# Optimization experiments

Measured on AMD Instinct MI355X. Metric: run time of the kernel, lower is better.

## Reference

```python
import jax, jax.numpy as jnp
import numpy as np

N_NODES = 50000
N_EDGES = 800000
IN_F = 191
H1, C1 = 16, 16   # conv1: heads=16, out=16, concat -> 256
H2, C2 = 8, 3     # conv2: heads=8, out=3, concat=False -> mean


def _glorot(key, shape):
    fan = shape[0] + shape[-1] if len(shape) == 2 else sum(shape)
    s = jnp.sqrt(6.0 / fan)
    return jax.random.uniform(key, shape, jnp.float32, -s, s)


def setup_inputs() -> dict:
    key = jax.random.key(0)
    ks = jax.random.split(key, 16)
    x = jax.random.normal(ks[0], (N_NODES, IN_F), jnp.float32)
    edge_index = jax.random.randint(ks[1], (2, N_EDGES), 0, N_NODES)
    edge_attr = jax.random.normal(ks[2], (N_EDGES, 1), jnp.float32)
    return {
        "x": x, "edge_index": edge_index, "edge_attr": edge_attr,
        "W1": _glorot(ks[3], (IN_F, H1 * C1)),
        "We1": _glorot(ks[4], (1, H1 * C1)),
        "a_src1": _glorot(ks[5], (H1, C1)),
        "a_dst1": _glorot(ks[6], (H1, C1)),
        "a_edge1": _glorot(ks[7], (H1, C1)),
        "b1": jnp.zeros((H1 * C1,), jnp.float32),
        "W2": _glorot(ks[8], (H1 * C1, H2 * C2)),
        "We2": _glorot(ks[9], (1, H2 * C2)),
        "a_src2": _glorot(ks[10], (H2, C2)),
        "a_dst2": _glorot(ks[11], (H2, C2)),
        "a_edge2": _glorot(ks[12], (H2, C2)),
        "b2": jnp.zeros((C2,), jnp.float32),
    }


def gat_conv(x, src, dst, edge_attr, W, We, a_src, a_dst, a_edge, bias, H, C, concat):
    # x: [N, F]; src/dst: [E'] (self loops already appended); edge_attr: [E', De]
    N = x.shape[0]
    xl = (x @ W).reshape(N, H, C)                       # [N,H,C]
    e = (edge_attr @ We).reshape(-1, H, C)              # [E',H,C]
    alpha_src = (xl * a_src).sum(-1)                    # [N,H]
    alpha_dst = (xl * a_dst).sum(-1)                    # [N,H]
    alpha_e = (e * a_edge).sum(-1)                      # [E',H]
    alpha = alpha_src[src] + alpha_dst[dst] + alpha_e   # [E',H]
    alpha = jax.nn.leaky_relu(alpha, 0.2)
    # softmax over incoming edges per destination node
    m = jax.ops.segment_max(alpha, dst, num_segments=N)
    alpha = jnp.exp(alpha - m[dst])
    den = jax.ops.segment_sum(alpha, dst, num_segments=N)
    alpha = alpha / (den[dst] + 1e-16)
    out = jax.ops.segment_sum(alpha[:, :, None] * xl[src], dst, num_segments=N)  # [N,H,C]
    if concat:
        return out.reshape(N, H * C) + bias
    return out.mean(axis=1) + bias


def reference(x, edge_index, edge_attr, W1, We1, a_src1, a_dst1, a_edge1, b1,
              W2, We2, a_src2, a_dst2, a_edge2, b2):
    N = x.shape[0]
    # add self loops (PyG default, edge_attr fill_value='mean')
    loop = jnp.arange(N)
    src = jnp.concatenate([edge_index[0], loop])
    dst = jnp.concatenate([edge_index[1], loop])
    ea_mean = edge_attr.mean(axis=0, keepdims=True)
    ea = jnp.concatenate([edge_attr, jnp.broadcast_to(ea_mean, (N, edge_attr.shape[1]))], axis=0)

    h = gat_conv(x, src, dst, ea, W1, We1, a_src1, a_dst1, a_edge1, b1, H1, C1, True)
    h = jax.nn.elu(h)
    h = gat_conv(h, src, dst, ea, W2, We2, a_src2, a_dst2, a_edge2, b2, H2, C2, False)
    h = jax.nn.elu(h)
    return h
```

## Files before the change

kernel.cpp:

```cpp
#include <hip/hip_runtime.h>
#include <math.h>
#include <stdint.h>

#define N_NODES 50000
#define N_EDGES 800000
#define N_TOT   850000
#define IN_F    191
#define F1      256
#define NH1     16
#define NC1     16
#define F2      24
#define NH2     8
#define NC2     3
#define KP      192
#define MPAD    50048
#define NCVT_X  (MPAD * 24)
#define NCVT_W  (F1 * 24)

typedef __attribute__((ext_vector_type(8))) short bf16x8;
typedef __attribute__((ext_vector_type(4))) float f32x4;

#define GLL16(g, s) __builtin_amdgcn_global_load_lds( \
    (const __attribute__((address_space(1))) void*)(g), \
    (__attribute__((address_space(3))) void*)(s), 16, 0, 0)

__device__ __forceinline__ float lrelu(float x) { return x > 0.f ? x : 0.2f * x; }

__device__ __forceinline__ uint16_t f2bf1(float f) {
    uint32_t u = __float_as_uint(f);
    return (uint16_t)((u + 0x7fffu + ((u >> 16) & 1u)) >> 16);
}
__device__ __forceinline__ void bf2f2(uint32_t u, float* lo, float* hi) {
    *lo = __uint_as_float(u << 16);
    *hi = __uint_as_float(u & 0xffff0000u);
}

__global__ void k_hist(const int* __restrict__ ei, int* counts) {
    int e = blockIdx.x * blockDim.x + threadIdx.x;
    if (e < N_EDGES) atomicAdd(&counts[ei[N_EDGES + e]], 1);
}

__global__ void k_easum(const float* __restrict__ ea, float* __restrict__ part) {
    __shared__ float wsums[4];
    int t = threadIdx.x;
    float v = 0.f;
    for (int e = blockIdx.x * 256 + t; e < N_EDGES; e += 256 * 256) v += ea[e];
    #pragma unroll
    for (int off = 32; off >= 1; off >>= 1) v += __shfl_xor(v, off);
    if ((t & 63) == 0) wsums[t >> 6] = v;
    __syncthreads();
    if (t == 0) part[blockIdx.x] = wsums[0] + wsums[1] + wsums[2] + wsums[3];
}

__global__ void k_wedot(const float* __restrict__ We1, const float* __restrict__ ae1,
                        const float* __restrict__ We2, const float* __restrict__ ae2,
                        const float* __restrict__ part, float* scalars) {
    int t = threadIdx.x;
    if (t < NH1) {
        float s = 0.f;
        for (int c = 0; c < NC1; c++) s += We1[t * NC1 + c] * ae1[t * NC1 + c];
        scalars[1 + t] = s;
    } else if (t < NH1 + NH2) {
        int h = t - NH1;
        float s = 0.f;
        for (int c = 0; c < NC2; c++) s += We2[h * NC2 + c] * ae2[h * NC2 + c];
        scalars[17 + h] = s;
    }
    float v = part[t * 4] + part[t * 4 + 1] + part[t * 4 + 2] + part[t * 4 + 3];
    #pragma unroll
    for (int off = 32; off >= 1; off >>= 1) v += __shfl_xor(v, off);
    if (t == 0) scalars[0] = v / (float)N_EDGES;
}

__global__ __launch_bounds__(1024) void k_scan1(const int* __restrict__ counts,
                                                int* rowptr, int* bsums) {
    __shared__ int wsum[16];
    int t = threadIdx.x;
    int lane = t & 63, w = t >> 6;
    int i = blockIdx.x * 1024 + t;
    int v = (i < N_NODES) ? counts[i] + 1 : 0;
    int incl = v;
    #pragma unroll
    for (int off = 1; off < 64; off <<= 1) {
        int u = __shfl_up(incl, off);
        if (lane >= off) incl += u;
    }
    if (lane == 63) wsum[w] = incl;
    __syncthreads();
    int woff = 0;
    #pragma unroll
    for (int k = 0; k < 16; k++) woff += (k < w) ? wsum[k] : 0;
    if (i < N_NODES) rowptr[i] = woff + incl - v;
    if (t == 1023) bsums[blockIdx.x] = woff + incl;
}

__global__ __launch_bounds__(1024) void k_scan2(int* rowptr, int* cursor,
                                                const int* __restrict__ bsums) {
    __shared__ int off_s;
    int b = blockIdx.x, t = threadIdx.x;
    if (t == 0) {
        int o = 0;
        for (int k = 0; k < b; k++) o += bsums[k];
        off_s = o;
        if (b == 48) rowptr[N_NODES] = o + bsums[48];
    }
    __syncthreads();
    int i = b * 1024 + t;
    if (i < N_NODES) {
        int r = rowptr[i] + off_s;
        rowptr[i] = r;
        cursor[i] = r;
    }
}

__global__ void k_scatter(const int* __restrict__ ei, const float* __restrict__ ea,
                          const float* __restrict__ scalars, int* cursor,
                          uint32_t* __restrict__ csr) {
    int i = blockIdx.x * blockDim.x + threadIdx.x;
    if (i < N_EDGES) {
        int s = ei[i], d = ei[N_EDGES + i];
        int pos = atomicAdd(&cursor[d], 1);
        csr[pos] = (uint32_t)s | ((uint32_t)f2bf1(ea[i]) << 16);
    } else if (i < N_TOT) {
        int n = i - N_EDGES;
        int pos = atomicAdd(&cursor[n], 1);
        csr[pos] = (uint32_t)n | ((uint32_t)f2bf1(scalars[0]) << 16);
    }
}

__global__ void k_cvt(const float* __restrict__ x, const float* __restrict__ W1,
                      uint16_t* __restrict__ xh, uint16_t* __restrict__ wht) {
    int idx = blockIdx.x * 256 + threadIdx.x;
    if (idx < NCVT_X) {
        int row = idx / 24, kw = idx - row * 24;
        int k0 = kw * 8;
        uint16_t hv[8];
        #pragma unroll
        for (int j = 0; j < 8; j++) {
            int k = k0 + j;
            float v = (row < N_NODES && k < IN_F) ? x[(size_t)row * IN_F + k] : 0.f;
            hv[j] = f2bf1(v);
        }
        *(uint4*)(xh + (size_t)row * KP + k0) = *(const uint4*)hv;
    } else if (idx < NCVT_X + NCVT_W) {
        int id2 = idx - NCVT_X;
        int col = id2 / 24, kw = id2 - col * 24;
        int k0 = kw * 8;
        uint16_t hv[8];
        #pragma unroll
        for (int j = 0; j < 8; j++) {
            int k = k0 + j;
            float v = (k < IN_F) ? W1[(size_t)k * F1 + col] : 0.f;
            hv[j] = f2bf1(v);
        }
        *(uint4*)(wht + (size_t)col * KP + k0) = *(const uint4*)hv;
    }
}

__global__ __launch_bounds__(256) void k_gemm1_mfma(const uint16_t* __restrict__ xh,
        const uint16_t* __restrict__ wht, uint16_t* __restrict__ xl1b) {
    __shared__ uint16_t ldsA[8 * 64 * 8];
    __shared__ uint16_t ldsB[8 * 64 * 8];
    const int t = threadIdx.x;
    const int l = t & 63, w = t >> 6;
    const int wm = w >> 1, wn = w & 1;
    const int m0 = blockIdx.x * 128;
    const int n0 = blockIdx.y * 128;
    const int lr = l & 15, lk = l >> 4;

    f32x4 acc[4][4];
    #pragma unroll
    for (int i = 0; i < 4; i++)
        #pragma unroll
        for (int j = 0; j < 4; j++)
            acc[i][j] = (f32x4){0.f, 0.f, 0.f, 0.f};

    for (int ks = 0; ks < 6; ks++) {
        const int kb = ks * 32 + lk * 8;
        #pragma unroll
        for (int ii = 0; ii < 4; ii++) {
            const int idx = w * 4 + ii;
            if (idx < 8) {
                const uint16_t* src = xh + (size_t)(m0 + idx * 16 + lr) * KP + kb;
                GLL16(src, ldsA + idx * 512);
            } else {
                const int g = idx - 8;
                const uint16_t* src = wht + (size_t)(n0 + g * 16 + lr) * KP + kb;
                GLL16(src, ldsB + g * 512);
            }
        }
        __syncthreads();
        bf16x8 ah[4];
        #pragma unroll
        for (int i = 0; i < 4; i++)
            ah[i] = *(const bf16x8*)(ldsA + ((wm * 4 + i) * 64 + l) * 8);
        #pragma unroll
        for (int j = 0; j < 4; j++) {
            bf16x8 bh = *(const bf16x8*)(ldsB + ((wn * 4 + j) * 64 + l) * 8);
            #pragma unroll
            for (int i = 0; i < 4; i++)
                acc[i][j] = __builtin_amdgcn_mfma_f32_16x16x32_bf16(ah[i], bh, acc[i][j], 0, 0, 0);
        }
        __syncthreads();
    }
    #pragma unroll
    for (int i = 0; i < 4; i++) {
        const int gm_base = m0 + wm * 64 + i * 16 + lk * 4;
        #pragma unroll
        for (int r = 0; r < 4; r++) {
            const int gm = gm_base + r;
            if (gm < N_NODES) {
                #pragma unroll
                for (int j = 0; j < 4; j++) {
                    const int gn = n0 + wn * 64 + j * 16 + lr;
                    xl1b[(size_t)gm * F1 + gn] = f2bf1(acc[i][j][r]);
                }
            }
        }
    }
}

__global__ void k_alphas1(const uint16_t* __restrict__ xl1b, const float* __restrict__ a_src,
                          const float* __restrict__ a_dst,
                          float* __restrict__ asrc, float* __restrict__ adst) {
    int idx = blockIdx.x * blockDim.x + threadIdx.x;
    if (idx >= N_NODES * NH1) return;
    int h = idx & 15;
    const uint4* xp = (const uint4*)(xl1b + (size_t)idx * 16);
    uint4 u0 = xp[0], u1 = xp[1];
    uint32_t us[8] = {u0.x, u0.y, u0.z, u0.w, u1.x, u1.y, u1.z, u1.w};
    float as = 0.f, ad = 0.f;
    #pragma unroll
    for (int q = 0; q < 8; q++) {
        float lo, hi;
        bf2f2(us[q], &lo, &hi);
        as += lo * a_src[h * 16 + 2 * q] + hi * a_src[h * 16 + 2 * q + 1];
        ad += lo * a_dst[h * 16 + 2 * q] + hi * a_dst[h * 16 + 2 * q + 1];
    }
    asrc[idx] = as;
    adst[idx] = ad;
}

__global__ __launch_bounds__(256) void k_agg1(const int* __restrict__ rowptr,
        const uint32_t* __restrict__ csr,
        const uint16_t* __restrict__ xl1b, const float* __restrict__ asrc,
        const float* __restrict__ adst, const float* __restrict__ scalars,
        const float* __restrict__ b1, uint16_t* __restrict__ h1b) {
    int node = blockIdx.x * 4 + (threadIdx.x >> 6);
    int lane = threadIdx.x & 63;
    int eg = lane >> 4, h = lane & 15;
    int r0 = rowptr[node], r1 = rowptr[node + 1];
    float ad = adst[node * 16 + h];
    float wd = scalars[1 + h];
    float den = 0.f;
    float acc[16];
    #pragma unroll
    for (int c = 0; c < 16; c++) acc[c] = 0.f;
    for (int j = r0 + eg; j < r1; j += 4) {
        uint32_t pk = csr[j];
        int s = (int)(pk & 0xFFFFu);
        float eav = __uint_as_float(pk & 0xFFFF0000u);
        float a = lrelu(asrc[s * 16 + h] + ad + eav * wd);
        float wgt = __expf(a);
        den += wgt;
        const uint4* xp = (const uint4*)(xl1b + (size_t)s * F1 + h * 16);
        uint4 u0 = xp[0], u1 = xp[1];
        float lo, hi;
        bf2f2(u0.x, &lo, &hi); acc[0] += wgt * lo;  acc[1] += wgt * hi;
        bf2f2(u0.y, &lo, &hi); acc[2] += wgt * lo;  acc[3] += wgt * hi;
        bf2f2(u0.z, &lo, &hi); acc[4] += wgt * lo;  acc[5] += wgt * hi;
        bf2f2(u0.w, &lo, &hi); acc[6] += wgt * lo;  acc[7] += wgt * hi;
        bf2f2(u1.x, &lo, &hi); acc[8] += wgt * lo;  acc[9] += wgt * hi;
        bf2f2(u1.y, &lo, &hi); acc[10] += wgt * lo; acc[11] += wgt * hi;
        bf2f2(u1.z, &lo, &hi); acc[12] += wgt * lo; acc[13] += wgt * hi;
        bf2f2(u1.w, &lo, &hi); acc[14] += wgt * lo; acc[15] += wgt * hi;
    }
    den += __shfl_xor(den, 16);
    den += __shfl_xor(den, 32);
    float inv = 1.f / (den + 1e-16f);
    #pragma unroll
    for (int c = 0; c < 16; c++) {
        acc[c] += __shfl_xor(acc[c], 16);
        acc[c] += __shfl_xor(acc[c], 32);
    }
    if (eg == 0) {
        uint32_t pk[8];
        #pragma unroll
        for (int q = 0; q < 8; q++) {
            float v0 = acc[2 * q] * inv + b1[h * 16 + 2 * q];
            float v1 = acc[2 * q + 1] * inv + b1[h * 16 + 2 * q + 1];
            v0 = v0 > 0.f ? v0 : expm1f(v0);
            v1 = v1 > 0.f ? v1 : expm1f(v1);
            pk[q] = (uint32_t)f2bf1(v0) | ((uint32_t)f2bf1(v1) << 16);
        }
        uint4* op = (uint4*)(h1b + (size_t)node * F1 + h * 16);
        op[0] = make_uint4(pk[0], pk[1], pk[2], pk[3]);
        op[1] = make_uint4(pk[4], pk[5], pk[6], pk[7]);
    }
}

__global__ __launch_bounds__(256) void k_layer2(const uint16_t* __restrict__ h1b,
        const float* __restrict__ W2, const float* __restrict__ a_src,
        const float* __restrict__ a_dst, uint16_t* __restrict__ xl2b,
        float* __restrict__ asrc, float* __restrict__ adst) {
    __shared__ float W2s[F2][258];
    int t = threadIdx.x;
    for (int i = t; i < 256 * F2; i += 256) {
        int k = i / F2, c = i - k * F2;
        W2s[c][k] = W2[i];
    }
    __syncthreads();
    int idx = blockIdx.x * 256 + t;
    if (idx >= N_NODES * NH2) return;
    int n = idx >> 3, h = idx & 7;
    int c0 = h * 3;
    const uint4* hp = (const uint4*)(h1b + (size_t)n * F1);
    float a0 = 0.f, a1 = 0.f, a2 = 0.f;
    #pragma unroll 4
    for (int q = 0; q < 32; q++) {
        uint4 u = hp[q];
        float f[8];
        bf2f2(u.x, &f[0], &f[1]);
        bf2f2(u.y, &f[2], &f[3]);
        bf2f2(u.z, &f[4], &f[5]);
        bf2f2(u.w, &f[6], &f[7]);
        #pragma unroll
        for (int j = 0; j < 8; j++) {
            int k = q * 8 + j;
            a0 += f[j] * W2s[c0][k];
            a1 += f[j] * W2s[c0 + 1][k];
            a2 += f[j] * W2s[c0 + 2][k];
        }
    }
    uint2 pk;
    pk.x = (uint32_t)f2bf1(a0) | ((uint32_t)f2bf1(a1) << 16);
    pk.y = (uint32_t)f2bf1(a2);
    *(uint2*)(xl2b + (size_t)idx * 4) = pk;
    asrc[idx] = a0 * a_src[h * 3 + 0] + a1 * a_src[h * 3 + 1] + a2 * a_src[h * 3 + 2];
    adst[idx] = a0 * a_dst[h * 3 + 0] + a1 * a_dst[h * 3 + 1] + a2 * a_dst[h * 3 + 2];
}

__global__ __launch_bounds__(256) void k_agg2(const int* __restrict__ rowptr,
        const uint32_t* __restrict__ csr,
        const uint16_t* __restrict__ xl2b, const float* __restrict__ asrc,
        const float* __restrict__ adst, const float* __restrict__ scalars,
        const float* __restrict__ b2, float* __restrict__ out) {
    int node = blockIdx.x * 4 + (threadIdx.x >> 6);
    int lane = threadIdx.x & 63;
    int eg = lane >> 3, h = lane & 7;
    int r0 = rowptr[node], r1 = rowptr[node + 1];
    float ad = adst[node * 8 + h];
    float wd = scalars[17 + h];
    float den = 0.f, a0 = 0.f, a1 = 0.f, a2 = 0.f;
    for (int j = r0 + eg; j < r1; j += 8) {
        uint32_t pk = csr[j];
        int s = (int)(pk & 0xFFFFu);
        float eav = __uint_as_float(pk & 0xFFFF0000u);
        float a = lrelu(asrc[s * 8 + h] + ad + eav * wd);
        float wgt = __expf(a);
        den += wgt;
        const uint2* xp = (const uint2*)(xl2b + ((size_t)s * 8 + h) * 4);
        uint2 u = xp[0];
        float x0, x1, x2, dummy;
        bf2f2(u.x, &x0, &x1);
        bf2f2(u.y, &x2, &dummy);
        a0 += wgt * x0;
        a1 += wgt * x1;
        a2 += wgt * x2;
    }
    den += __shfl_xor(den, 8); den += __shfl_xor(den, 16); den += __shfl_xor(den, 32);
    float inv = 1.f / (den + 1e-16f);
    a0 += __shfl_xor(a0, 8); a0 += __shfl_xor(a0, 16); a0 += __shfl_xor(a0, 32);
    a1 += __shfl_xor(a1, 8); a1 += __shfl_xor(a1, 16); a1 += __shfl_xor(a1, 32);
    a2 += __shfl_xor(a2, 8); a2 += __shfl_xor(a2, 16); a2 += __shfl_xor(a2, 32);
    a0 *= inv; a1 *= inv; a2 *= inv;
    a0 += __shfl_xor(a0, 1); a0 += __shfl_xor(a0, 2); a0 += __shfl_xor(a0, 4);
    a1 += __shfl_xor(a1, 1); a1 += __shfl_xor(a1, 2); a1 += __shfl_xor(a1, 4);
    a2 += __shfl_xor(a2, 1); a2 += __shfl_xor(a2, 2); a2 += __shfl_xor(a2, 4);
    if (lane == 0) {
        float v0 = a0 * 0.125f + b2[0];
        float v1 = a1 * 0.125f + b2[1];
        float v2 = a2 * 0.125f + b2[2];
        out[node * 3 + 0] = v0 > 0.f ? v0 : expm1f(v0);
        out[node * 3 + 1] = v1 > 0.f ? v1 : expm1f(v1);
        out[node * 3 + 2] = v2 > 0.f ? v2 : expm1f(v2);
    }
}

extern "C" void kernel_launch(void* const* d_in, const int* in_sizes, int n_in,
                              void* d_out, int out_size, void* d_ws, size_t ws_size,
                              hipStream_t stream) {
    const float* x       = (const float*)d_in[0];
    const int*   ei      = (const int*)d_in[1];
    const float* ea      = (const float*)d_in[2];
    const float* W1      = (const float*)d_in[3];
    const float* We1     = (const float*)d_in[4];
    const float* a_src1  = (const float*)d_in[5];
    const float* a_dst1  = (const float*)d_in[6];
    const float* a_edge1 = (const float*)d_in[7];
    const float* b1      = (const float*)d_in[8];
    const float* W2      = (const float*)d_in[9];
    const float* We2     = (const float*)d_in[10];
    const float* a_src2  = (const float*)d_in[11];
    const float* a_dst2  = (const float*)d_in[12];
    const float* a_edge2 = (const float*)d_in[13];
    const float* b2      = (const float*)d_in[14];
    float* out = (float*)d_out;

    char* ws = (char*)d_ws;
    size_t off = 0;
    auto alloc = [&](size_t nbytes) -> void* {
        void* p = ws + off;
        off = (off + nbytes + 255) & ~(size_t)255;
        return p;
    };
    uint16_t* xl1b  = (uint16_t*)alloc((size_t)N_NODES * F1 * 2);
    uint16_t* h1b   = (uint16_t*)alloc((size_t)N_NODES * F1 * 2);
    float* asrc1    = (float*)alloc((size_t)N_NODES * NH1 * 4);
    float* adst1    = (float*)alloc((size_t)N_NODES * NH1 * 4);
    uint16_t* xl2b  = (uint16_t*)alloc((size_t)N_NODES * 32 * 2);
    float* asrc2    = (float*)alloc((size_t)N_NODES * NH2 * 4);
    float* adst2    = (float*)alloc((size_t)N_NODES * NH2 * 4);
    int*   counts   = (int*)alloc((size_t)N_NODES * 4);
    int*   rowptr   = (int*)alloc((size_t)(N_NODES + 1) * 4);
    int*   cursor   = (int*)alloc((size_t)N_NODES * 4);
    int*   bsums    = (int*)alloc(64 * 4);
    uint32_t* csr   = (uint32_t*)alloc((size_t)N_TOT * 4);
    float* scalars  = (float*)alloc(128);
    float* part     = (float*)alloc(256 * 4);
    uint16_t* wht   = (uint16_t*)alloc((size_t)F1 * KP * 2);
    uint16_t* xh    = (uint16_t*)alloc((size_t)MPAD * KP * 2);

    hipMemsetAsync(counts, 0, (size_t)N_NODES * 4, stream);
    hipLaunchKernelGGL(k_hist, dim3((N_EDGES + 255) / 256), dim3(256), 0, stream,
                       ei, counts);
    hipLaunchKernelGGL(k_easum, dim3(256), dim3(256), 0, stream, ea, part);
    hipLaunchKernelGGL(k_wedot, dim3(1), dim3(64), 0, stream,
                       We1, a_edge1, We2, a_edge2, part, scalars);
    hipLaunchKernelGGL(k_scan1, dim3(49), dim3(1024), 0, stream, counts, rowptr, bsums);
    hipLaunchKernelGGL(k_scan2, dim3(49), dim3(1024), 0, stream, rowptr, cursor, bsums);
    hipLaunchKernelGGL(k_scatter, dim3((N_TOT + 255) / 256), dim3(256), 0, stream,
                       ei, ea, scalars, cursor, csr);
    hipLaunchKernelGGL(k_cvt, dim3((NCVT_X + NCVT_W + 255) / 256), dim3(256), 0, stream,
                       x, W1, xh, wht);
    hipLaunchKernelGGL(k_gemm1_mfma, dim3(MPAD / 128, 2), dim3(256), 0, stream,
                       xh, wht, xl1b);
    hipLaunchKernelGGL(k_alphas1, dim3((N_NODES * NH1 + 255) / 256), dim3(256), 0, stream,
                       xl1b, a_src1, a_dst1, asrc1, adst1);
    hipLaunchKernelGGL(k_agg1, dim3(N_NODES / 4), dim3(256), 0, stream,
                       rowptr, csr, xl1b, asrc1, adst1, scalars, b1, h1b);
    hipLaunchKernelGGL(k_layer2, dim3((N_NODES * NH2 + 255) / 256), dim3(256), 0, stream,
                       h1b, W2, a_src2, a_dst2, xl2b, asrc2, adst2);
    hipLaunchKernelGGL(k_agg2, dim3(N_NODES / 4), dim3(256), 0, stream,
                       rowptr, csr, xl2b, asrc2, adst2, scalars, b2, out);
}
```

Before: 296.3 us.

## Fuse preprocessing kernels and fold attention-logit computation into GEMM epilogue

Merges the histogram, edge-attr sum and bf16 conversion kernels into one launch. It also folds the scalar We·a_edge and mean computation into an extra block of the scan kernel. The GEMM is retiled to 64 rows by the full 256 columns per block, so each block holds whole node rows. The tile is staged in LDS so the per-head source/destination attention dots are computed in the epilogue, which removes the separate k_alphas1 pass that re-read xl1b. This cuts launch count and global traffic, at the cost of 32KB of LDS per block and a different GEMM tile shape that may lower occupancy.

```diff
diff --git a/kernel.cpp b/kernel.cpp
--- a/kernel.cpp
+++ b/kernel.cpp
@@ -16,6 +16,9 @@
 #define MPAD    50048
 #define NCVT_X  (MPAD * 24)
 #define NCVT_W  (F1 * 24)
+#define HIST_B  3125
+#define EASUM_B 256
+#define CVT_B   ((NCVT_X + NCVT_W) / 256)
 
 typedef __attribute__((ext_vector_type(8))) short bf16x8;
 typedef __attribute__((ext_vector_type(4))) float f32x4;
@@ -35,49 +38,81 @@
     *hi = __uint_as_float(u & 0xffff0000u);
 }
 
-__global__ void k_hist(const int* __restrict__ ei, int* counts) {
-    int e = blockIdx.x * blockDim.x + threadIdx.x;
-    if (e < N_EDGES) atomicAdd(&counts[ei[N_EDGES + e]], 1);
-}
-
-__global__ void k_easum(const float* __restrict__ ea, float* __restrict__ part) {
-    __shared__ float wsums[4];
-    int t = threadIdx.x;
-    float v = 0.f;
-    for (int e = blockIdx.x * 256 + t; e < N_EDGES; e += 256 * 256) v += ea[e];
-    #pragma unroll
-    for (int off = 32; off >= 1; off >>= 1) v += __shfl_xor(v, off);
-    if ((t & 63) == 0) wsums[t >> 6] = v;
-    __syncthreads();
-    if (t == 0) part[blockIdx.x] = wsums[0] + wsums[1] + wsums[2] + wsums[3];
-}
-
-__global__ void k_wedot(const float* __restrict__ We1, const float* __restrict__ ae1,
-                        const float* __restrict__ We2, const float* __restrict__ ae2,
-                        const float* __restrict__ part, float* scalars) {
-    int t = threadIdx.x;
-    if (t < NH1) {
-        float s = 0.f;
-        for (int c = 0; c < NC1; c++) s += We1[t * NC1 + c] * ae1[t * NC1 + c];
-        scalars[1 + t] = s;
-    } else if (t < NH1 + NH2) {
-        int h = t - NH1;
-        float s = 0.f;
-        for (int c = 0; c < NC2; c++) s += We2[h * NC2 + c] * ae2[h * NC2 + c];
-        scalars[17 + h] = s;
-    }
-    float v = part[t * 4] + part[t * 4 + 1] + part[t * 4 + 2] + part[t * 4 + 3];
-    #pragma unroll
-    for (int off = 32; off >= 1; off >>= 1) v += __shfl_xor(v, off);
-    if (t == 0) scalars[0] = v / (float)N_EDGES;
+__global__ void k_pre(const int* __restrict__ ei, const float* __restrict__ ea,
+                      const float* __restrict__ x, const float* __restrict__ W1,
+                      int* counts, float* __restrict__ part,
+                      uint16_t* __restrict__ xh, uint16_t* __restrict__ wht) {
+    int b = blockIdx.x, t = threadIdx.x;
+    if (b < HIST_B) {
+        int e = b * 256 + t;
+        if (e < N_EDGES) atomicAdd(&counts[ei[N_EDGES + e]], 1);
+    } else if (b < HIST_B + EASUM_B) {
+        __shared__ float wsums[4];
+        int eb = b - HIST_B;
+        float v = 0.f;
+        for (int e = eb * 256 + t; e < N_EDGES; e += 256 * 256) v += ea[e];
+        #pragma unroll
+        for (int off = 32; off >= 1; off >>= 1) v += __shfl_xor(v, off);
+        if ((t & 63) == 0) wsums[t >> 6] = v;
+        __syncthreads();
+        if (t == 0) part[eb] = wsums[0] + wsums[1] + wsums[2] + wsums[3];
+    } else {
+        int idx = (b - HIST_B - EASUM_B) * 256 + t;
+        if (idx < NCVT_X) {
+            int row = idx / 24, kw = idx - row * 24;
+            int k0 = kw * 8;
+            uint16_t hv[8];
+            #pragma unroll
+            for (int j = 0; j < 8; j++) {
+                int k = k0 + j;
+                float v = (row < N_NODES && k < IN_F) ? x[(size_t)row * IN_F + k] : 0.f;
+                hv[j] = f2bf1(v);
+            }
+            *(uint4*)(xh + (size_t)row * KP + k0) = *(const uint4*)hv;
+        } else {
+            int id2 = idx - NCVT_X;
+            int col = id2 / 24, kw = id2 - col * 24;
+            int k0 = kw * 8;
+            uint16_t hv[8];
+            #pragma unroll
+            for (int j = 0; j < 8; j++) {
+                int k = k0 + j;
+                float v = (k < IN_F) ? W1[(size_t)k * F1 + col] : 0.f;
+                hv[j] = f2bf1(v);
+            }
+            *(uint4*)(wht + (size_t)col * KP + k0) = *(const uint4*)hv;
+        }
+    }
 }
 
 __global__ __launch_bounds__(1024) void k_scan1(const int* __restrict__ counts,
-                                                int* rowptr, int* bsums) {
+        int* rowptr, int* bsums,
+        const float* __restrict__ We1, const float* __restrict__ ae1,
+        const float* __restrict__ We2, const float* __restrict__ ae2,
+        const float* __restrict__ part, float* scalars) {
+    int b = blockIdx.x, t = threadIdx.x;
+    if (b == 49) {
+        if (t < 64) {
+            if (t < NH1) {
+                float s = 0.f;
+                for (int c = 0; c < NC1; c++) s += We1[t * NC1 + c] * ae1[t * NC1 + c];
+                scalars[1 + t] = s;
+            } else if (t < NH1 + NH2) {
+                int h = t - NH1;
+                float s = 0.f;
+                for (int c = 0; c < NC2; c++) s += We2[h * NC2 + c] * ae2[h * NC2 + c];
+                scalars[17 + h] = s;
+            }
+            float v = part[t * 4] + part[t * 4 + 1] + part[t * 4 + 2] + part[t * 4 + 3];
+            #pragma unroll
+            for (int off = 32; off >= 1; off >>= 1) v += __shfl_xor(v, off);
+            if (t == 0) scalars[0] = v / (float)N_EDGES;
+        }
+        return;
+    }
     __shared__ int wsum[16];
-    int t = threadIdx.x;
     int lane = t & 63, w = t >> 6;
-    int i = blockIdx.x * 1024 + t;
+    int i = b * 1024 + t;
     int v = (i < N_NODES) ? counts[i] + 1 : 0;
     int incl = v;
     #pragma unroll
@@ -91,7 +126,7 @@
     #pragma unroll
     for (int k = 0; k < 16; k++) woff += (k < w) ? wsum[k] : 0;
     if (i < N_NODES) rowptr[i] = woff + incl - v;
-    if (t == 1023) bsums[blockIdx.x] = woff + incl;
+    if (t == 1023) bsums[b] = woff + incl;
 }
 
 __global__ __launch_bounds__(1024) void k_scan2(int* rowptr, int* cursor,
@@ -128,44 +163,16 @@
     }
 }
 
-__global__ void k_cvt(const float* __restrict__ x, const float* __restrict__ W1,
-                      uint16_t* __restrict__ xh, uint16_t* __restrict__ wht) {
-    int idx = blockIdx.x * 256 + threadIdx.x;
-    if (idx < NCVT_X) {
-        int row = idx / 24, kw = idx - row * 24;
-        int k0 = kw * 8;
-        uint16_t hv[8];
-        #pragma unroll
-        for (int j = 0; j < 8; j++) {
-            int k = k0 + j;
-            float v = (row < N_NODES && k < IN_F) ? x[(size_t)row * IN_F + k] : 0.f;
-            hv[j] = f2bf1(v);
-        }
-        *(uint4*)(xh + (size_t)row * KP + k0) = *(const uint4*)hv;
-    } else if (idx < NCVT_X + NCVT_W) {
-        int id2 = idx - NCVT_X;
-        int col = id2 / 24, kw = id2 - col * 24;
-        int k0 = kw * 8;
-        uint16_t hv[8];
-        #pragma unroll
-        for (int j = 0; j < 8; j++) {
-            int k = k0 + j;
-            float v = (k < IN_F) ? W1[(size_t)k * F1 + col] : 0.f;
-            hv[j] = f2bf1(v);
-        }
-        *(uint4*)(wht + (size_t)col * KP + k0) = *(const uint4*)hv;
-    }
-}
-
 __global__ __launch_bounds__(256) void k_gemm1_mfma(const uint16_t* __restrict__ xh,
-        const uint16_t* __restrict__ wht, uint16_t* __restrict__ xl1b) {
-    __shared__ uint16_t ldsA[8 * 64 * 8];
-    __shared__ uint16_t ldsB[8 * 64 * 8];
+        const uint16_t* __restrict__ wht, const float* __restrict__ a_src,
+        const float* __restrict__ a_dst, uint16_t* __restrict__ xl1b,
+        float* __restrict__ asrc1, float* __restrict__ adst1) {
+    __shared__ uint16_t smem[64 * 256];
+    uint16_t* ldsA = smem;
+    uint16_t* ldsB = smem + 4 * 512;
     const int t = threadIdx.x;
     const int l = t & 63, w = t >> 6;
-    const int wm = w >> 1, wn = w & 1;
-    const int m0 = blockIdx.x * 128;
-    const int n0 = blockIdx.y * 128;
+    const int m0 = blockIdx.x * 64;
     const int lr = l & 15, lk = l >> 4;
 
     f32x4 acc[4][4];
@@ -178,14 +185,14 @@
     for (int ks = 0; ks < 6; ks++) {
         const int kb = ks * 32 + lk * 8;
         #pragma unroll
-        for (int ii = 0; ii < 4; ii++) {
-            const int idx = w * 4 + ii;
-            if (idx < 8) {
+        for (int ii = 0; ii < 5; ii++) {
+            const int idx = w * 5 + ii;
+            if (idx < 4) {
                 const uint16_t* src = xh + (size_t)(m0 + idx * 16 + lr) * KP + kb;
                 GLL16(src, ldsA + idx * 512);
             } else {
-                const int g = idx - 8;
-                const uint16_t* src = wht + (size_t)(n0 + g * 16 + lr) * KP + kb;
+                const int g = idx - 4;
+                const uint16_t* src = wht + (size_t)(g * 16 + lr) * KP + kb;
                 GLL16(src, ldsB + g * 512);
             }
         }
@@ -193,10 +200,11 @@
         bf16x8 ah[4];
         #pragma unroll
         for (int i = 0; i < 4; i++)
-            ah[i] = *(const bf16x8*)(ldsA + ((wm * 4 + i) * 64 + l) * 8);
+            ah[i] = *(const bf16x8*)(ldsA + (i * 64 + l) * 8);
         #pragma unroll
         for (int j = 0; j < 4; j++) {
-            bf16x8 bh = *(const bf16x8*)(ldsB + ((wn * 4 + j) * 64 + l) * 8);
+            const int g = w * 4 + j;
+            bf16x8 bh = *(const bf16x8*)(ldsB + (g * 64 + l) * 8);
             #pragma unroll
             for (int i = 0; i < 4; i++)
                 acc[i][j] = __builtin_amdgcn_mfma_f32_16x16x32_bf16(ah[i], bh, acc[i][j], 0, 0, 0);
@@ -205,40 +213,41 @@
     }
     #pragma unroll
     for (int i = 0; i < 4; i++) {
-        const int gm_base = m0 + wm * 64 + i * 16 + lk * 4;
         #pragma unroll
         for (int r = 0; r < 4; r++) {
-            const int gm = gm_base + r;
-            if (gm < N_NODES) {
-                #pragma unroll
-                for (int j = 0; j < 4; j++) {
-                    const int gn = n0 + wn * 64 + j * 16 + lr;
-                    xl1b[(size_t)gm * F1 + gn] = f2bf1(acc[i][j][r]);
-                }
-            }
-        }
-    }
-}
-
-__global__ void k_alphas1(const uint16_t* __restrict__ xl1b, const float* __restrict__ a_src,
-                          const float* __restrict__ a_dst,
-                          float* __restrict__ asrc, float* __restrict__ adst) {
-    int idx = blockIdx.x * blockDim.x + threadIdx.x;
-    if (idx >= N_NODES * NH1) return;
-    int h = idx & 15;
-    const uint4* xp = (const uint4*)(xl1b + (size_t)idx * 16);
-    uint4 u0 = xp[0], u1 = xp[1];
-    uint32_t us[8] = {u0.x, u0.y, u0.z, u0.w, u1.x, u1.y, u1.z, u1.w};
-    float as = 0.f, ad = 0.f;
-    #pragma unroll
-    for (int q = 0; q < 8; q++) {
-        float lo, hi;
-        bf2f2(us[q], &lo, &hi);
-        as += lo * a_src[h * 16 + 2 * q] + hi * a_src[h * 16 + 2 * q + 1];
-        ad += lo * a_dst[h * 16 + 2 * q] + hi * a_dst[h * 16 + 2 * q + 1];
-    }
-    asrc[idx] = as;
-    adst[idx] = ad;
+            const int lrow = i * 16 + lk * 4 + r;
+            const int gm = m0 + lrow;
+            #pragma unroll
+            for (int j = 0; j < 4; j++) {
+                const int gn = (w * 4 + j) * 16 + lr;
+                uint16_t bv = f2bf1(acc[i][j][r]);
+                smem[lrow * 256 + gn] = bv;
+                if (gm < N_NODES) xl1b[(size_t)gm * F1 + gn] = bv;
+            }
+        }
+    }
+    __syncthreads();
+    #pragma unroll
+    for (int q = 0; q < 4; q++) {
+        int item = q * 256 + t;
+        int row = item >> 4, h = item & 15;
+        int gm = m0 + row;
+        if (gm < N_NODES) {
+            const uint4* rp = (const uint4*)(smem + row * 256 + h * 16);
+            uint4 u0 = rp[0], u1 = rp[1];
+            uint32_t us[8] = {u0.x, u0.y, u0.z, u0.w, u1.x, u1.y, u1.z, u1.w};
+            float as = 0.f, ad = 0.f;
+            #pragma unroll
+            for (int p = 0; p < 8; p++) {
+                float lo, hi;
+                bf2f2(us[p], &lo, &hi);
+                as += lo * a_src[h * 16 + 2 * p] + hi * a_src[h * 16 + 2 * p + 1];
+                ad += lo * a_dst[h * 16 + 2 * p] + hi * a_dst[h * 16 + 2 * p + 1];
+            }
+            asrc1[gm * 16 + h] = as;
+            adst1[gm * 16 + h] = ad;
+        }
+    }
 }
 
 __global__ __launch_bounds__(256) void k_agg1(const int* __restrict__ rowptr,
@@ -432,21 +441,15 @@
     uint16_t* xh    = (uint16_t*)alloc((size_t)MPAD * KP * 2);
 
     hipMemsetAsync(counts, 0, (size_t)N_NODES * 4, stream);
-    hipLaunchKernelGGL(k_hist, dim3((N_EDGES + 255) / 256), dim3(256), 0, stream,
-                       ei, counts);
-    hipLaunchKernelGGL(k_easum, dim3(256), dim3(256), 0, stream, ea, part);
-    hipLaunchKernelGGL(k_wedot, dim3(1), dim3(64), 0, stream,
-                       We1, a_edge1, We2, a_edge2, part, scalars);
-    hipLaunchKernelGGL(k_scan1, dim3(49), dim3(1024), 0, stream, counts, rowptr, bsums);
+    hipLaunchKernelGGL(k_pre, dim3(HIST_B + EASUM_B + CVT_B), dim3(256), 0, stream,
+                       ei, ea, x, W1, counts, part, xh, wht);
+    hipLaunchKernelGGL(k_scan1, dim3(50), dim3(1024), 0, stream,
+                       counts, rowptr, bsums, We1, a_edge1, We2, a_edge2, part, scalars);
     hipLaunchKernelGGL(k_scan2, dim3(49), dim3(1024), 0, stream, rowptr, cursor, bsums);
     hipLaunchKernelGGL(k_scatter, dim3((N_TOT + 255) / 256), dim3(256), 0, stream,
                        ei, ea, scalars, cursor, csr);
-    hipLaunchKernelGGL(k_cvt, dim3((NCVT_X + NCVT_W + 255) / 256), dim3(256), 0, stream,
-                       x, W1, xh, wht);
-    hipLaunchKernelGGL(k_gemm1_mfma, dim3(MPAD / 128, 2), dim3(256), 0, stream,
-                       xh, wht, xl1b);
-    hipLaunchKernelGGL(k_alphas1, dim3((N_NODES * NH1 + 255) / 256), dim3(256), 0, stream,
-                       xl1b, a_src1, a_dst1, asrc1, adst1);
+    hipLaunchKernelGGL(k_gemm1_mfma, dim3(MPAD / 64), dim3(256), 0, stream,
+                       xh, wht, a_src1, a_dst1, xl1b, asrc1, adst1);
     hipLaunchKernelGGL(k_agg1, dim3(N_NODES / 4), dim3(256), 0, stream,
                        rowptr, csr, xl1b, asrc1, adst1, scalars, b1, h1b);
     hipLaunchKernelGGL(k_layer2, dim3((N_NODES * NH2 + 255) / 256), dim3(256), 0, stream,
```

Result: faster. 275.2 us (-7.1%).
